# Kernel tuning notes

Hardware: AMD Instinct MI355X
Metric: run time of the kernel (lower is better)

The kernel has to match this reference:

```python
import jax, jax.numpy as jnp
import numpy as np

VAR_NUM, IN_DIM, OUT_DIM = 3, 8, 32
N_PTS, M_PTS, K_LAST = 8192, 2048, 10
RADIUS = 0.0342
PROJ_HIDDEN = 64
N_DIM = 2
MLP_DIMS = [2 * N_DIM + OUT_DIM, 80, 80, OUT_DIM]  # [36, 80, 80, 32]


def _gelu(x):
    # torch F.gelu default = exact erf form
    return jax.nn.gelu(x, approximate=False)


def _radius_neighbors(data, queries, r):
    # CSR-style neighbor lists (indices grouped per query), chunked for memory
    idx_chunks = []
    counts = np.zeros(queries.shape[0], np.int64)
    r2 = r * r
    for s in range(0, queries.shape[0], 1024):
        q = queries[s:s + 1024]
        d2 = ((q[:, None, :] - data[None, :, :]) ** 2).sum(-1)
        mask = d2 <= r2
        _, cols = np.nonzero(mask)  # row-major -> grouped by query
        idx_chunks.append(cols.astype(np.int32))
        counts[s:s + q.shape[0]] = mask.sum(1)
    return np.concatenate(idx_chunks), counts.astype(np.int32)


def _knn(data, queries, k):
    out = np.zeros((queries.shape[0], k), np.int32)
    for s in range(0, queries.shape[0], 1024):
        q = queries[s:s + 1024]
        d2 = ((q[:, None, :] - data[None, :, :]) ** 2).sum(-1)
        out[s:s + q.shape[0]] = np.argpartition(d2, k, axis=1)[:, :k]
    return out.reshape(-1)


def _mlp_params(key, dims):
    Ws, bs = [], []
    for i in range(len(dims) - 1):
        key, k1 = jax.random.split(key)
        Ws.append(jax.random.normal(k1, (dims[i], dims[i + 1]), jnp.float32) / np.sqrt(dims[i]).astype(np.float32))
        bs.append(jnp.zeros((dims[i + 1],), jnp.float32))
    return Ws, bs


def setup_inputs():
    rng = np.random.default_rng(0)
    input_grid = rng.uniform(size=(N_PTS, N_DIM)).astype(np.float32)
    output_grid = rng.uniform(size=(M_PTS, N_DIM)).astype(np.float32)
    nbr_index, nbr_counts = _radius_neighbors(input_grid, input_grid, RADIUS)
    nbr_seg = np.repeat(np.arange(N_PTS, dtype=np.int32), nbr_counts)
    nbr_last_index = _knn(input_grid, output_grid, K_LAST)

    key = jax.random.key(0)
    ks = jax.random.split(key, 4)
    inp = jax.random.normal(ks[0], (1, N_PTS, VAR_NUM * IN_DIM), jnp.float32)
    pW, pb = _mlp_params(ks[1], [IN_DIM, PROJ_HIDDEN, OUT_DIM])
    it0_W, it0_b = _mlp_params(ks[2], MLP_DIMS)
    it1_W, it1_b = _mlp_params(ks[3], MLP_DIMS)
    return dict(
        inp=inp,
        input_grid=jnp.asarray(input_grid), output_grid=jnp.asarray(output_grid),
        proj_W0=pW[0], proj_b0=pb[0], proj_W1=pW[1], proj_b1=pb[1],
        it0_W0=it0_W[0], it0_b0=it0_b[0], it0_W1=it0_W[1], it0_b1=it0_b[1], it0_W2=it0_W[2], it0_b2=it0_b[2],
        it1_W0=it1_W[0], it1_b0=it1_b[0], it1_W1=it1_W[1], it1_b1=it1_b[1], it1_W2=it1_W[2], it1_b2=it1_b[2],
        nbr_index=jnp.asarray(nbr_index), nbr_seg=jnp.asarray(nbr_seg),
        nbr_counts=jnp.asarray(nbr_counts), nbr_last_index=jnp.asarray(nbr_last_index),
    )


def _mlp3(x, W0, b0, W1, b1, W2, b2):
    x = _gelu(x @ W0 + b0)
    x = _gelu(x @ W1 + b1)
    return x @ W2 + b2


def reference(inp, input_grid, output_grid, proj_W0, proj_b0, proj_W1, proj_b1,
              it0_W0, it0_b0, it0_W1, it0_b1, it0_W2, it0_b2,
              it1_W0, it1_b0, it1_W1, it1_b1, it1_W2, it1_b2,
              nbr_index, nbr_seg, nbr_counts, nbr_last_index):
    B, N, _ = inp.shape  # B must be 1 (module's IT indexing assumes it)
    x = inp.reshape(B * N, VAR_NUM, IN_DIM)
    # pointwise projection MLP (gelu between layers)
    x = _gelu(x @ proj_W0 + proj_b0) @ proj_W1 + proj_b1  # (N, V, OUT_DIM)

    inv_counts = (1.0 / jnp.maximum(nbr_counts, 1).astype(x.dtype))[:, None]
    y_pos = input_grid[nbr_index]        # (E, 2) neighbor positions
    self_pos = input_grid[nbr_seg]       # (E, 2) query positions
    last_y = input_grid[nbr_last_index]                    # (M*K, 2)
    last_self = jnp.repeat(output_grid, K_LAST, axis=0)    # (M*K, 2)

    outs = []
    for v in range(VAR_NUM):
        f = x[:, v, :]
        # IT layer 0: radius neighborhoods on input grid, residual add
        agg = jnp.concatenate([y_pos, self_pos, f[nbr_index]], axis=-1)  # (E, 36)
        h = _mlp3(agg, it0_W0, it0_b0, it0_W1, it0_b1, it0_W2, it0_b2)
        f = jax.ops.segment_sum(h, nbr_seg, num_segments=N) * inv_counts + f
        # IT layer 1 (last): fixed-K neighbors from input grid to output grid, mean
        agg = jnp.concatenate([last_y, last_self, f[nbr_last_index]], axis=-1)
        h = _mlp3(agg, it1_W0, it1_b0, it1_W1, it1_b1, it1_W2, it1_b2)
        outs.append(h.reshape(M_PTS, K_LAST, OUT_DIM).mean(axis=1))
    # original concatenates temp[None] along dim=2 -> (1, M, V*OUT_DIM)
    return jnp.concatenate(outs, axis=-1)[None]
```

## Files before the change

kernel.cpp:

```cpp
#include <hip/hip_runtime.h>
#include <hip/hip_bf16.h>
#include <math.h>

#define N_PTS 8192
#define M_PTS 2048
#define KLAST 10
#define VARS 3
#define OUTD 32
#define D1 80
#define D2 80
#define PB 8
#define LPTS 4
#define NT 512
#define NWAVES 8
#define NTL 256
#define NWL 4
#define TPCH 104
#define RP 32

#define FRAG 512
#define W0F 10
#define W1F 15
#define W2F 6
#define WPACK ((W0F + W1F + W2F) * FRAG)

typedef float f4 __attribute__((ext_vector_type(4)));
typedef short bf16x8 __attribute__((ext_vector_type(8)));

__device__ __forceinline__ float gelu_f(float x) {
    float x2 = x * x;
    float s = x * __builtin_fmaf(0.1029418f, x2, 2.3022083f);
    float u = __builtin_amdgcn_exp2f(s);
    float r = __builtin_amdgcn_rcpf(u + 1.0f);
    return __builtin_fmaf(-x, r, x);
}
__device__ __forceinline__ unsigned short f2bf(float x) {
    unsigned int u = __float_as_uint(x);
    u += 0x7FFF + ((u >> 16) & 1);
    return (unsigned short)(u >> 16);
}
__device__ __forceinline__ float bf2f(unsigned short h) {
    return __uint_as_float(((unsigned int)h) << 16);
}
__device__ __forceinline__ int pk2(float a, float b) {
    __hip_bfloat162 h = __float22bfloat162_rn(float2{a, b});
    int r; __builtin_memcpy(&r, &h, 4); return r;
}

__device__ __forceinline__ void pack_weights(
    const float* __restrict__ W0g, const float* __restrict__ W1g,
    const float* __restrict__ W2g, unsigned short* __restrict__ wp, int t)
{
    for (int idx = t; idx < W0F * FRAG; idx += 256) {
        int f = idx >> 9, r = idx & 511;
        int lane = r >> 3, e = r & 7;
        int lm = lane & 15, quad = lane >> 4;
        int cb = f >> 1, ks = f & 1;
        int col = cb * 16 + lm;
        int k = ks * 32 + quad * 8 + e;
        float w = (k < 32) ? W0g[(k + 4) * D1 + col]
                           : ((k < 36) ? W0g[(k - 32) * D1 + col] : 0.0f);
        wp[idx] = f2bf(w);
    }
    for (int idx = t; idx < W1F * FRAG; idx += 256) {
        int f = idx >> 9, r = idx & 511;
        int lane = r >> 3, e = r & 7;
        int lm = lane & 15, quad = lane >> 4;
        int cb = f / 3, ks = f - cb * 3;
        int col = cb * 16 + lm;
        int k = ks * 32 + quad * 8 + e;
        wp[W0F * FRAG + idx] = f2bf((k < D2) ? W1g[k * D1 + col] : 0.0f);
    }
    for (int idx = t; idx < W2F * FRAG; idx += 256) {
        int f = idx >> 9, r = idx & 511;
        int lane = r >> 3, e = r & 7;
        int lm = lane & 15, quad = lane >> 4;
        int cb = f / 3, ks = f - cb * 3;
        int col = cb * 16 + lm;
        int k = ks * 32 + quad * 8 + e;
        wp[(W0F + W1F) * FRAG + idx] = f2bf((k < D2) ? W2g[k * OUTD + col] : 0.0f);
    }
}

__device__ __forceinline__ void mlp_chunk(
    int4 featsi, int4 posfi, unsigned short* Trow,
    const unsigned short* __restrict__ Wl,
    const float* bs, int lm, int quad)
{
    bf16x8 b1f0 = *(bf16x8*)&featsi;
    bf16x8 b1f1 = *(bf16x8*)&posfi;
#pragma unroll 1
    for (int cb = 0; cb < 5; ++cb) {
        f4 acc = *(const f4*)&bs[cb * 16 + quad * 4];
        bf16x8 a0 = *(const bf16x8*)&Wl[(cb * 2 + 0) * FRAG];
        bf16x8 a1 = *(const bf16x8*)&Wl[(cb * 2 + 1) * FRAG];
        acc = __builtin_amdgcn_mfma_f32_16x16x32_bf16(a0, b1f0, acc, 0, 0, 0);
        acc = __builtin_amdgcn_mfma_f32_16x16x32_bf16(a1, b1f1, acc, 0, 0, 0);
        *(int2*)&Trow[cb * 16 + quad * 4] =
            make_int2(pk2(gelu_f(acc.x), gelu_f(acc.y)),
                      pk2(gelu_f(acc.z), gelu_f(acc.w)));
    }
    bf16x8 b2f[3];
    b2f[0] = *(const bf16x8*)&Trow[quad * 8];
    b2f[1] = *(const bf16x8*)&Trow[32 + quad * 8];
    b2f[2] = *(const bf16x8*)&Trow[64 + quad * 8];
#pragma unroll 1
    for (int cb = 0; cb < 5; ++cb) {
        f4 acc = *(const f4*)&bs[80 + cb * 16 + quad * 4];
        const unsigned short* wh = &Wl[(W0F + cb * 3) * FRAG];
        bf16x8 h0 = *(const bf16x8*)&wh[0];
        bf16x8 h1 = *(const bf16x8*)&wh[FRAG];
        bf16x8 h2 = *(const bf16x8*)&wh[2 * FRAG];
        acc = __builtin_amdgcn_mfma_f32_16x16x32_bf16(h0, b2f[0], acc, 0, 0, 0);
        acc = __builtin_amdgcn_mfma_f32_16x16x32_bf16(h1, b2f[1], acc, 0, 0, 0);
        acc = __builtin_amdgcn_mfma_f32_16x16x32_bf16(h2, b2f[2], acc, 0, 0, 0);
        *(int2*)&Trow[cb * 16 + quad * 4] =
            make_int2(pk2(gelu_f(acc.x), gelu_f(acc.y)),
                      pk2(gelu_f(acc.z), gelu_f(acc.w)));
    }
    bf16x8 b3f[3];
    b3f[0] = *(const bf16x8*)&Trow[quad * 8];
    b3f[1] = *(const bf16x8*)&Trow[32 + quad * 8];
    b3f[2] = *(const bf16x8*)&Trow[64 + quad * 8];
    float* po = (float*)Trow;
#pragma unroll 1
    for (int cb = 0; cb < 2; ++cb) {
        f4 acc = *(const f4*)&bs[160 + cb * 16 + quad * 4];
        const unsigned short* wh = &Wl[(W0F + W1F + cb * 3) * FRAG];
        bf16x8 h0 = *(const bf16x8*)&wh[0];
        bf16x8 h1 = *(const bf16x8*)&wh[FRAG];
        bf16x8 h2 = *(const bf16x8*)&wh[2 * FRAG];
        acc = __builtin_amdgcn_mfma_f32_16x16x32_bf16(h0, b3f[0], acc, 0, 0, 0);
        acc = __builtin_amdgcn_mfma_f32_16x16x32_bf16(h1, b3f[1], acc, 0, 0, 0);
        acc = __builtin_amdgcn_mfma_f32_16x16x32_bf16(h2, b3f[2], acc, 0, 0, 0);
        *(f4*)&po[cb * 16 + quad * 4] = acc;
    }
}

__global__ __launch_bounds__(256) void proj_scan_kernel(
    const float* __restrict__ inp, const float* __restrict__ grid_in,
    const float* __restrict__ W0, const float* __restrict__ b0,
    const float* __restrict__ W1, const float* __restrict__ b1,
    unsigned short* __restrict__ f0b, int* __restrict__ posb,
    const int* __restrict__ counts, int* __restrict__ offsets,
    const float* __restrict__ i0W0, const float* __restrict__ i0W1,
    const float* __restrict__ i0W2, unsigned short* __restrict__ wpack0,
    const float* __restrict__ i1W0, const float* __restrict__ i1W1,
    const float* __restrict__ i1W2, unsigned short* __restrict__ wpack1)
{
    const int t = threadIdx.x;
    if (blockIdx.x == 769) { pack_weights(i0W0, i0W1, i0W2, wpack0, t); return; }
    if (blockIdx.x == 770) { pack_weights(i1W0, i1W1, i1W2, wpack1, t); return; }
    if (blockIdx.x == 768) {
        __shared__ int ws2[4], wx2[4];
        const int lane = t & 63, wave = t >> 6;
        int4 a[8];
#pragma unroll
        for (int i = 0; i < 8; ++i) a[i] = ((const int4*)counts)[t * 8 + i];
        int s = 0;
#pragma unroll
        for (int i = 0; i < 8; ++i) s += a[i].x + a[i].y + a[i].z + a[i].w;
        int x = s;
#pragma unroll
        for (int d = 1; d < 64; d <<= 1) {
            int y = __shfl_up(x, d);
            if (lane >= d) x += y;
        }
        if (lane == 63) ws2[wave] = x;
        __syncthreads();
        if (t == 0) {
            wx2[0] = 0;
            wx2[1] = ws2[0];
            wx2[2] = ws2[0] + ws2[1];
            wx2[3] = ws2[0] + ws2[1] + ws2[2];
        }
        __syncthreads();
        int base = wx2[wave] + (x - s);
#pragma unroll
        for (int i = 0; i < 8; ++i) {
            int4 c = a[i];
            int4 o;
            o.x = base; base += c.x;
            o.y = base; base += c.y;
            o.z = base; base += c.z;
            o.w = base; base += c.w;
            ((int4*)offsets)[t * 8 + i] = o;
        }
        return;
    }
    __shared__ float W0s[8 * 64];
    __shared__ float W1s[64 * OUTD];
    __shared__ float xs[32 * 8];
    __shared__ float H[32 * 64];
    const int r0 = blockIdx.x * 32;
    for (int idx = t; idx < 512; idx += 256) W0s[idx] = W0[idx];
    for (int idx = t; idx < 64 * OUTD; idx += 256) W1s[idx] = W1[idx];
    xs[t] = inp[r0 * 8 + t];
    if (t < 32) {
        int row = r0 + t, n = row / 3;
        posb[n] = pk2(grid_in[2 * n], grid_in[2 * n + 1]);
    }
    __syncthreads();
#pragma unroll 1
    for (int p = 0; p < 8; ++p) {
        int o = t + 256 * p, r = o >> 6, col = o & 63;
        float s = b0[col];
#pragma unroll
        for (int k = 0; k < 8; ++k) s += xs[r * 8 + k] * W0s[k * 64 + col];
        H[o] = gelu_f(s);
    }
    __syncthreads();
#pragma unroll 1
    for (int p = 0; p < 4; ++p) {
        int o = t + 256 * p, r = o >> 5, c = o & 31;
        float s = b1[c];
#pragma unroll 8
        for (int k = 0; k < 64; ++k) s += H[r * 64 + k] * W1s[k * OUTD + c];
        int row = r0 + r;
        int n = row / 3, v = row - n * 3;
        f0b[((size_t)(v << 13) + n) * RP + c] = f2bf(s);
    }
}

__global__ __launch_bounds__(512, 8) void agg_kernel(
    const float* __restrict__ grid_in, const unsigned short* __restrict__ f0b,
    const int* __restrict__ posb,
    const int* __restrict__ nbr_index, const int* __restrict__ offsets,
    const int* __restrict__ counts,
    const unsigned short* __restrict__ wpack,
    const float* __restrict__ b0g, const float* __restrict__ b1g,
    const float* __restrict__ b2g,
    unsigned short* __restrict__ f1b)
{
    __shared__ __attribute__((aligned(16))) unsigned short Tb[NWAVES * 16 * TPCH];
    __shared__ __attribute__((aligned(16))) float bs[192];
    __shared__ __attribute__((aligned(16))) float accH[VARS * PB * 32];
    __shared__ int offs[PB + 1];
    __shared__ int px2b[PB];
    __shared__ float invb[PB];

    const int t = threadIdx.x;
    const int lane = t & 63, wave = t >> 6;
    const int lm = lane & 15, quad = lane >> 4;
    const int p0 = blockIdx.x * PB;
    const unsigned short* Wl = wpack + lane * 8;

    for (int idx = t; idx < 192; idx += NT)
        bs[idx] = (idx < 80) ? b0g[idx] : (idx < 160 ? b1g[idx - 80] : b2g[idx - 160]);
    if (t < PB) {
        offs[t] = offsets[p0 + t];
        int c = counts[p0 + t];
        invb[t] = 1.0f / (float)(c > 1 ? c : 1);
        px2b[t] = pk2(grid_in[2 * (p0 + t)], grid_in[2 * (p0 + t) + 1]);
    }
    if (t == PB) offs[PB] = offsets[p0 + PB - 1] + counts[p0 + PB - 1];
    for (int idx = t; idx < VARS * PB * 32; idx += NT) accH[idx] = 0.0f;
    __syncthreads();

    unsigned short* TbW = Tb + (wave * 16) * TPCH;
    if (lane < 32)
        *(int4*)(TbW + (lane >> 1) * TPCH + 80 + (lane & 1) * 8) = make_int4(0, 0, 0, 0);

    const int e0 = offs[0];
    const int cntT = offs[PB] - e0;
    const int Rb = VARS * cntT;
    const int nch = (Rb + 15) >> 4;

    unsigned short* Trow = TbW + lm * TPCH;

    auto fetch_index = [&](int ch2, int& key, int& j) {
        key = -1; j = 0;
        if (ch2 < nch) {
            int myrow = (ch2 << 4) + lm;
            if (myrow < Rb) {
                int myv = (myrow >= 2 * cntT) ? 2 : ((myrow >= cntT) ? 1 : 0);
                int e = e0 + myrow - myv * cntT;
                int lp = 0;
#pragma unroll
                for (int l = 1; l < PB; ++l) lp += (e >= offs[l]);
                key = myv * PB + lp;
                j = nbr_index[e];
            }
        }
    };
    auto fetch_record = [&](int key, int j, int4& feats, int4& posf) {
        feats = make_int4(0, 0, 0, 0); posf = make_int4(0, 0, 0, 0);
        if (key >= 0) {
            int v = key >> 3, lp = key & 7;
            feats = ((const int4*)(f0b + ((size_t)(v << 13) + j) * RP))[quad];
            if (quad == 0) posf = make_int4(posb[j], px2b[lp], 0, 0);
        }
    };

    int keyA, jA, keyB, jB;
    fetch_index(wave, keyA, jA);
    fetch_index(wave + NWAVES, keyB, jB);
    int4 featsA, posfA;
    fetch_record(keyA, jA, featsA, posfA);

    for (int ch = wave; ch < nch; ch += NWAVES) {
        int ckey = keyA; int4 cf = featsA, cp = posfA;
        keyA = keyB; jA = jB;
        fetch_index(ch + 2 * NWAVES, keyB, jB);
        fetch_record(keyA, jA, featsA, posfA);
        mlp_chunk(cf, cp, Trow, Wl, bs, lm, quad);
        int col = lane & 31, eo = lane >> 5;
#pragma unroll 1
        for (int e2 = eo; e2 < 16; e2 += 2) {
            int k = __shfl(ckey, e2);
            if (k >= 0)
                atomicAdd(&accH[k * 32 + col], ((const float*)(TbW + e2 * TPCH))[col]);
        }
    }
    __syncthreads();
    for (int idx = t; idx < VARS * PB * OUTD; idx += NT) {
        int key = idx >> 5, c = idx & 31;
        int v = key >> 3, lp = key & 7;
        size_t rec = ((size_t)(v << 13) + p0 + lp) * RP;
        float val = accH[key * 32 + c] * invb[lp] + bf2f(f0b[rec + c]);
        f1b[rec + c] = f2bf(val);
    }
}

__global__ __launch_bounds__(256, 8) void last_kernel(
    const unsigned short* __restrict__ f1b, const int* __restrict__ posb,
    const float* __restrict__ grid_out,
    const int* __restrict__ nbr_last,
    const unsigned short* __restrict__ wpack,
    const float* __restrict__ b0g, const float* __restrict__ b1g,
    const float* __restrict__ b2g,
    float* __restrict__ out)
{
    __shared__ __attribute__((aligned(16))) unsigned short Tb[NWL * 16 * TPCH];
    __shared__ __attribute__((aligned(16))) float bs[192];
    __shared__ __attribute__((aligned(16))) float accH[LPTS * VARS * 32];
    __shared__ int pxo2b[LPTS];

    const int t = threadIdx.x;
    const int lane = t & 63, wave = t >> 6;
    const int lm = lane & 15, quad = lane >> 4;
    const int m0 = blockIdx.x * LPTS;
    const unsigned short* Wl = wpack + lane * 8;

    for (int idx = t; idx < 192; idx += NTL)
        bs[idx] = (idx < 80) ? b0g[idx] : (idx < 160 ? b1g[idx - 80] : b2g[idx - 160]);
    if (t < LPTS)
        pxo2b[t] = pk2(grid_out[2 * (m0 + t)], grid_out[2 * (m0 + t) + 1]);
    for (int idx = t; idx < LPTS * VARS * 32; idx += NTL) accH[idx] = 0.0f;
    __syncthreads();
    unsigned short* TbW = Tb + (wave * 16) * TPCH;
    if (lane < 32)
        *(int4*)(TbW + (lane >> 1) * TPCH + 80 + (lane & 1) * 8) = make_int4(0, 0, 0, 0);

    const int Rb = LPTS * VARS * KLAST;
    const int nch = (Rb + 15) >> 4;
    unsigned short* Trow = TbW + lm * TPCH;

    auto fetch_index = [&](int ch2, int& key, int& j) {
        key = -1; j = 0;
        if (ch2 < nch) {
            int myrow = (ch2 << 4) + lm;
            if (myrow < Rb) {
                int lp = myrow / 30, rr = myrow - lp * 30;
                int v = rr / KLAST, kk = rr - v * KLAST;
                j = nbr_last[(m0 + lp) * KLAST + kk];
                key = lp * VARS + v;
            }
        }
    };
    auto fetch_record = [&](int key, int j, int4& feats, int4& posf) {
        feats = make_int4(0, 0, 0, 0); posf = make_int4(0, 0, 0, 0);
        if (key >= 0) {
            int lp = key / VARS, v = key - lp * VARS;
            feats = ((const int4*)(f1b + ((size_t)(v << 13) + j) * RP))[quad];
            if (quad == 0) posf = make_int4(posb[j], pxo2b[lp], 0, 0);
        }
    };

    int keyA, jA, keyB, jB;
    fetch_index(wave, keyA, jA);
    fetch_index(wave + NWL, keyB, jB);
    int4 featsA, posfA;
    fetch_record(keyA, jA, featsA, posfA);

    for (int ch = wave; ch < nch; ch += NWL) {
        int ckey = keyA; int4 cf = featsA, cp = posfA;
        keyA = keyB; jA = jB;
        fetch_index(ch + 2 * NWL, keyB, jB);
        fetch_record(keyA, jA, featsA, posfA);
        mlp_chunk(cf, cp, Trow, Wl, bs, lm, quad);
        int col = lane & 31, eo = lane >> 5;
#pragma unroll 1
        for (int e2 = eo; e2 < 16; e2 += 2) {
            int k = __shfl(ckey, e2);
            if (k >= 0)
                atomicAdd(&accH[k * 32 + col], ((const float*)(TbW + e2 * TPCH))[col]);
        }
    }
    __syncthreads();
    for (int idx = t; idx < LPTS * VARS * OUTD; idx += NTL) {
        int key = idx >> 5, c = idx & 31;
        int lp = key / VARS, v = key - lp * VARS;
        out[((size_t)(m0 + lp) * VARS + v) * OUTD + c] = accH[key * 32 + c] * (1.0f / KLAST);
    }
}

extern "C" void kernel_launch(void* const* d_in, const int* in_sizes, int n_in,
                              void* d_out, int out_size, void* d_ws, size_t ws_size,
                              hipStream_t stream) {
    const float* inp      = (const float*)d_in[0];
    const float* grid_in  = (const float*)d_in[1];
    const float* grid_out = (const float*)d_in[2];
    const float* pW0 = (const float*)d_in[3];
    const float* pb0 = (const float*)d_in[4];
    const float* pW1 = (const float*)d_in[5];
    const float* pb1 = (const float*)d_in[6];
    const float* i0W0 = (const float*)d_in[7];
    const float* i0b0 = (const float*)d_in[8];
    const float* i0W1 = (const float*)d_in[9];
    const float* i0b1 = (const float*)d_in[10];
    const float* i0W2 = (const float*)d_in[11];
    const float* i0b2 = (const float*)d_in[12];
    const float* i1W0 = (const float*)d_in[13];
    const float* i1b0 = (const float*)d_in[14];
    const float* i1W1 = (const float*)d_in[15];
    const float* i1b1 = (const float*)d_in[16];
    const float* i1W2 = (const float*)d_in[17];
    const float* i1b2 = (const float*)d_in[18];
    const int* nbr_index  = (const int*)d_in[19];
    const int* nbr_counts = (const int*)d_in[21];
    const int* nbr_last   = (const int*)d_in[22];

    unsigned short* f0b = (unsigned short*)d_ws;
    unsigned short* f1b = f0b + (size_t)VARS * N_PTS * RP;
    int* offsets = (int*)(f1b + (size_t)VARS * N_PTS * RP);
    int* posb    = offsets + N_PTS;
    unsigned short* wpack0 = (unsigned short*)(posb + N_PTS);
    unsigned short* wpack1 = wpack0 + WPACK;

    proj_scan_kernel<<<771, 256, 0, stream>>>(inp, grid_in, pW0, pb0, pW1, pb1,
                                              f0b, posb, nbr_counts, offsets,
                                              i0W0, i0W1, i0W2, wpack0,
                                              i1W0, i1W1, i1W2, wpack1);
    agg_kernel<<<N_PTS / PB, NT, 0, stream>>>(grid_in, f0b, posb, nbr_index, offsets,
                                              nbr_counts, wpack0,
                                              i0b0, i0b1, i0b2, f1b);
    last_kernel<<<M_PTS / LPTS, NTL, 0, stream>>>(f1b, posb, grid_out, nbr_last, wpack1,
                                                  i1b0, i1b1, i1b2,
                                                  (float*)d_out);
}
```

Measured before the change: 308.9 us.

## Keep MLP activations in registers and stage packed weights in LDS

The MLP chunk no longer round-trips layer activations through an LDS scratch tile. The weight packing order is permuted so each MFMA output fragment maps directly onto the next layer's B-operand registers. The final layer atomically adds its accumulator straight into a transposed, padded shared accumulator, replacing the shuffle-and-atomic loop. Packed weights are copied into LDS per block instead of being read from global memory, and the output kernel now handles 2 points per block instead of 4. In exchange, every block pays a larger LDS footprint and a weight copy, which may reduce occupancy.

```diff
diff --git a/kernel.cpp b/kernel.cpp
--- a/kernel.cpp
+++ b/kernel.cpp
@@ -10,12 +10,11 @@
 #define D1 80
 #define D2 80
 #define PB 8
-#define LPTS 4
+#define LPTS 2
 #define NT 512
 #define NWAVES 8
 #define NTL 256
 #define NWL 4
-#define TPCH 104
 #define RP 32
 
 #define FRAG 512
@@ -23,6 +22,11 @@
 #define W1F 15
 #define W2F 6
 #define WPACK ((W0F + W1F + W2F) * FRAG)
+
+#define AKEYS (VARS * PB)
+#define AKP   (AKEYS + 1)
+#define LKEYS (LPTS * VARS)
+#define LKP   (LKEYS + 1)
 
 typedef float f4 __attribute__((ext_vector_type(4)));
 typedef short bf16x8 __attribute__((ext_vector_type(8)));
@@ -45,6 +49,10 @@
 __device__ __forceinline__ int pk2(float a, float b) {
     __hip_bfloat162 h = __float22bfloat162_rn(float2{a, b});
     int r; __builtin_memcpy(&r, &h, 4); return r;
+}
+__device__ __forceinline__ bf16x8 mk8(int a, int b, int c, int d) {
+    int4 v = make_int4(a, b, c, d);
+    bf16x8 r; __builtin_memcpy(&r, &v, 16); return r;
 }
 
 __device__ __forceinline__ void pack_weights(
@@ -54,10 +62,10 @@
     for (int idx = t; idx < W0F * FRAG; idx += 256) {
         int f = idx >> 9, r = idx & 511;
         int lane = r >> 3, e = r & 7;
-        int lm = lane & 15, quad = lane >> 4;
+        int lm = lane & 15, qd = lane >> 4;
         int cb = f >> 1, ks = f & 1;
         int col = cb * 16 + lm;
-        int k = ks * 32 + quad * 8 + e;
+        int k = ks * 32 + qd * 8 + e;
         float w = (k < 32) ? W0g[(k + 4) * D1 + col]
                            : ((k < 36) ? W0g[(k - 32) * D1 + col] : 0.0f);
         wp[idx] = f2bf(w);
@@ -65,76 +73,87 @@
     for (int idx = t; idx < W1F * FRAG; idx += 256) {
         int f = idx >> 9, r = idx & 511;
         int lane = r >> 3, e = r & 7;
-        int lm = lane & 15, quad = lane >> 4;
+        int lm = lane & 15, qd = lane >> 4;
         int cb = f / 3, ks = f - cb * 3;
         int col = cb * 16 + lm;
-        int k = ks * 32 + quad * 8 + e;
-        wp[W0F * FRAG + idx] = f2bf((k < D2) ? W1g[k * D1 + col] : 0.0f);
+        int blk = 2 * ks + (e >> 2);
+        int srow = blk * 16 + qd * 4 + (e & 3);
+        wp[W0F * FRAG + idx] = f2bf((blk < 5) ? W1g[srow * D1 + col] : 0.0f);
     }
     for (int idx = t; idx < W2F * FRAG; idx += 256) {
         int f = idx >> 9, r = idx & 511;
         int lane = r >> 3, e = r & 7;
-        int lm = lane & 15, quad = lane >> 4;
+        int lm = lane & 15, qd = lane >> 4;
         int cb = f / 3, ks = f - cb * 3;
         int col = cb * 16 + lm;
-        int k = ks * 32 + quad * 8 + e;
-        wp[(W0F + W1F) * FRAG + idx] = f2bf((k < D2) ? W2g[k * OUTD + col] : 0.0f);
-    }
-}
+        int blk = 2 * ks + (e >> 2);
+        int srow = blk * 16 + qd * 4 + (e & 3);
+        wp[(W0F + W1F) * FRAG + idx] = f2bf((blk < 5) ? W2g[srow * OUTD + col] : 0.0f);
+    }
+}
+
+#define MFMA16(A, B, C) __builtin_amdgcn_mfma_f32_16x16x32_bf16(A, B, C, 0, 0, 0)
+#define GPACK(ACC) make_int2(pk2(gelu_f(ACC.x), gelu_f(ACC.y)), \
+                             pk2(gelu_f(ACC.z), gelu_f(ACC.w)))
 
 __device__ __forceinline__ void mlp_chunk(
-    int4 featsi, int4 posfi, unsigned short* Trow,
-    const unsigned short* __restrict__ Wl,
-    const float* bs, int lm, int quad)
+    int4 featsi, int2 posfi,
+    const unsigned short* WA, const float* bs,
+    int quad, int ckey, float* accH, int kp)
 {
-    bf16x8 b1f0 = *(bf16x8*)&featsi;
-    bf16x8 b1f1 = *(bf16x8*)&posfi;
-#pragma unroll 1
-    for (int cb = 0; cb < 5; ++cb) {
-        f4 acc = *(const f4*)&bs[cb * 16 + quad * 4];
-        bf16x8 a0 = *(const bf16x8*)&Wl[(cb * 2 + 0) * FRAG];
-        bf16x8 a1 = *(const bf16x8*)&Wl[(cb * 2 + 1) * FRAG];
-        acc = __builtin_amdgcn_mfma_f32_16x16x32_bf16(a0, b1f0, acc, 0, 0, 0);
-        acc = __builtin_amdgcn_mfma_f32_16x16x32_bf16(a1, b1f1, acc, 0, 0, 0);
-        *(int2*)&Trow[cb * 16 + quad * 4] =
-            make_int2(pk2(gelu_f(acc.x), gelu_f(acc.y)),
-                      pk2(gelu_f(acc.z), gelu_f(acc.w)));
-    }
-    bf16x8 b2f[3];
-    b2f[0] = *(const bf16x8*)&Trow[quad * 8];
-    b2f[1] = *(const bf16x8*)&Trow[32 + quad * 8];
-    b2f[2] = *(const bf16x8*)&Trow[64 + quad * 8];
-#pragma unroll 1
-    for (int cb = 0; cb < 5; ++cb) {
-        f4 acc = *(const f4*)&bs[80 + cb * 16 + quad * 4];
-        const unsigned short* wh = &Wl[(W0F + cb * 3) * FRAG];
-        bf16x8 h0 = *(const bf16x8*)&wh[0];
-        bf16x8 h1 = *(const bf16x8*)&wh[FRAG];
-        bf16x8 h2 = *(const bf16x8*)&wh[2 * FRAG];
-        acc = __builtin_amdgcn_mfma_f32_16x16x32_bf16(h0, b2f[0], acc, 0, 0, 0);
-        acc = __builtin_amdgcn_mfma_f32_16x16x32_bf16(h1, b2f[1], acc, 0, 0, 0);
-        acc = __builtin_amdgcn_mfma_f32_16x16x32_bf16(h2, b2f[2], acc, 0, 0, 0);
-        *(int2*)&Trow[cb * 16 + quad * 4] =
-            make_int2(pk2(gelu_f(acc.x), gelu_f(acc.y)),
-                      pk2(gelu_f(acc.z), gelu_f(acc.w)));
-    }
-    bf16x8 b3f[3];
-    b3f[0] = *(const bf16x8*)&Trow[quad * 8];
-    b3f[1] = *(const bf16x8*)&Trow[32 + quad * 8];
-    b3f[2] = *(const bf16x8*)&Trow[64 + quad * 8];
-    float* po = (float*)Trow;
-#pragma unroll 1
-    for (int cb = 0; cb < 2; ++cb) {
-        f4 acc = *(const f4*)&bs[160 + cb * 16 + quad * 4];
-        const unsigned short* wh = &Wl[(W0F + W1F + cb * 3) * FRAG];
-        bf16x8 h0 = *(const bf16x8*)&wh[0];
-        bf16x8 h1 = *(const bf16x8*)&wh[FRAG];
-        bf16x8 h2 = *(const bf16x8*)&wh[2 * FRAG];
-        acc = __builtin_amdgcn_mfma_f32_16x16x32_bf16(h0, b3f[0], acc, 0, 0, 0);
-        acc = __builtin_amdgcn_mfma_f32_16x16x32_bf16(h1, b3f[1], acc, 0, 0, 0);
-        acc = __builtin_amdgcn_mfma_f32_16x16x32_bf16(h2, b3f[2], acc, 0, 0, 0);
-        *(f4*)&po[cb * 16 + quad * 4] = acc;
-    }
+    bf16x8 b1f0; __builtin_memcpy(&b1f0, &featsi, 16);
+    int4 pv = make_int4(posfi.x, posfi.y, 0, 0);
+    bf16x8 b1f1; __builtin_memcpy(&b1f1, &pv, 16);
+
+    int2 k0, k1, k2, k3, k4;
+#define L1S(CB, PK) { \
+    f4 acc = *(const f4*)&bs[(CB) * 16 + quad * 4]; \
+    bf16x8 a0 = *(const bf16x8*)&WA[((CB) * 2 + 0) * FRAG]; \
+    bf16x8 a1 = *(const bf16x8*)&WA[((CB) * 2 + 1) * FRAG]; \
+    acc = MFMA16(a0, b1f0, acc); \
+    acc = MFMA16(a1, b1f1, acc); \
+    PK = GPACK(acc); }
+    L1S(0, k0) L1S(1, k1) L1S(2, k2) L1S(3, k3) L1S(4, k4)
+#undef L1S
+
+    bf16x8 b20 = mk8(k0.x, k0.y, k1.x, k1.y);
+    bf16x8 b21 = mk8(k2.x, k2.y, k3.x, k3.y);
+    bf16x8 b22 = mk8(k4.x, k4.y, 0, 0);
+    int2 q0, q1, q2, q3, q4;
+#define L2S(CB, QK) { \
+    f4 acc = *(const f4*)&bs[80 + (CB) * 16 + quad * 4]; \
+    const unsigned short* wh = &WA[(W0F + (CB) * 3) * FRAG]; \
+    bf16x8 h0 = *(const bf16x8*)&wh[0]; \
+    bf16x8 h1 = *(const bf16x8*)&wh[FRAG]; \
+    bf16x8 h2 = *(const bf16x8*)&wh[2 * FRAG]; \
+    acc = MFMA16(h0, b20, acc); \
+    acc = MFMA16(h1, b21, acc); \
+    acc = MFMA16(h2, b22, acc); \
+    QK = GPACK(acc); }
+    L2S(0, q0) L2S(1, q1) L2S(2, q2) L2S(3, q3) L2S(4, q4)
+#undef L2S
+
+    bf16x8 b30 = mk8(q0.x, q0.y, q1.x, q1.y);
+    bf16x8 b31 = mk8(q2.x, q2.y, q3.x, q3.y);
+    bf16x8 b32 = mk8(q4.x, q4.y, 0, 0);
+#define L3S(CB) { \
+    f4 acc = *(const f4*)&bs[160 + (CB) * 16 + quad * 4]; \
+    const unsigned short* wh = &WA[(W0F + W1F + (CB) * 3) * FRAG]; \
+    bf16x8 h0 = *(const bf16x8*)&wh[0]; \
+    bf16x8 h1 = *(const bf16x8*)&wh[FRAG]; \
+    bf16x8 h2 = *(const bf16x8*)&wh[2 * FRAG]; \
+    acc = MFMA16(h0, b30, acc); \
+    acc = MFMA16(h1, b31, acc); \
+    acc = MFMA16(h2, b32, acc); \
+    if (ckey >= 0) { \
+        float* ap = accH + ((CB) * 16 + quad * 4) * kp + ckey; \
+        atomicAdd(&ap[0], acc.x); \
+        atomicAdd(&ap[kp], acc.y); \
+        atomicAdd(&ap[2 * kp], acc.z); \
+        atomicAdd(&ap[3 * kp], acc.w); \
+    } }
+    L3S(0) L3S(1)
+#undef L3S
 }
 
 __global__ __launch_bounds__(256) void proj_scan_kernel(
@@ -232,18 +251,22 @@
     const float* __restrict__ b2g,
     unsigned short* __restrict__ f1b)
 {
-    __shared__ __attribute__((aligned(16))) unsigned short Tb[NWAVES * 16 * TPCH];
+    __shared__ __attribute__((aligned(16))) unsigned short Wls[WPACK];
     __shared__ __attribute__((aligned(16))) float bs[192];
-    __shared__ __attribute__((aligned(16))) float accH[VARS * PB * 32];
+    __shared__ __attribute__((aligned(16))) float accH[OUTD * AKP];
     __shared__ int offs[PB + 1];
     __shared__ int px2b[PB];
     __shared__ float invb[PB];
 
     const int t = threadIdx.x;
-    const int lane = t & 63, wave = t >> 6;
+    const int lane = t & 63;
     const int lm = lane & 15, quad = lane >> 4;
+    const int wave = t >> 6;
     const int p0 = blockIdx.x * PB;
-    const unsigned short* Wl = wpack + lane * 8;
+
+    for (int idx = t; idx < WPACK / 8; idx += NT)
+        ((int4*)Wls)[idx] = ((const int4*)wpack)[idx];
+    const unsigned short* WA = Wls + lane * 8;
 
     for (int idx = t; idx < 192; idx += NT)
         bs[idx] = (idx < 80) ? b0g[idx] : (idx < 160 ? b1g[idx - 80] : b2g[idx - 160]);
@@ -254,19 +277,13 @@
         px2b[t] = pk2(grid_in[2 * (p0 + t)], grid_in[2 * (p0 + t) + 1]);
     }
     if (t == PB) offs[PB] = offsets[p0 + PB - 1] + counts[p0 + PB - 1];
-    for (int idx = t; idx < VARS * PB * 32; idx += NT) accH[idx] = 0.0f;
-    __syncthreads();
-
-    unsigned short* TbW = Tb + (wave * 16) * TPCH;
-    if (lane < 32)
-        *(int4*)(TbW + (lane >> 1) * TPCH + 80 + (lane & 1) * 8) = make_int4(0, 0, 0, 0);
+    for (int idx = t; idx < OUTD * AKP; idx += NT) accH[idx] = 0.0f;
+    __syncthreads();
 
     const int e0 = offs[0];
     const int cntT = offs[PB] - e0;
     const int Rb = VARS * cntT;
     const int nch = (Rb + 15) >> 4;
-
-    unsigned short* Trow = TbW + lm * TPCH;
 
     auto fetch_index = [&](int ch2, int& key, int& j) {
         key = -1; j = 0;
@@ -283,41 +300,34 @@
             }
         }
     };
-    auto fetch_record = [&](int key, int j, int4& feats, int4& posf) {
-        feats = make_int4(0, 0, 0, 0); posf = make_int4(0, 0, 0, 0);
+    auto fetch_record = [&](int key, int j, int4& feats, int2& posf) {
+        feats = make_int4(0, 0, 0, 0); posf = make_int2(0, 0);
         if (key >= 0) {
             int v = key >> 3, lp = key & 7;
             feats = ((const int4*)(f0b + ((size_t)(v << 13) + j) * RP))[quad];
-            if (quad == 0) posf = make_int4(posb[j], px2b[lp], 0, 0);
+            if (quad == 0) posf = make_int2(posb[j], px2b[lp]);
         }
     };
 
     int keyA, jA, keyB, jB;
     fetch_index(wave, keyA, jA);
     fetch_index(wave + NWAVES, keyB, jB);
-    int4 featsA, posfA;
+    int4 featsA; int2 posfA;
     fetch_record(keyA, jA, featsA, posfA);
 
     for (int ch = wave; ch < nch; ch += NWAVES) {
-        int ckey = keyA; int4 cf = featsA, cp = posfA;
+        int ckey = keyA; int4 cf = featsA; int2 cp = posfA;
         keyA = keyB; jA = jB;
         fetch_index(ch + 2 * NWAVES, keyB, jB);
         fetch_record(keyA, jA, featsA, posfA);
-        mlp_chunk(cf, cp, Trow, Wl, bs, lm, quad);
-        int col = lane & 31, eo = lane >> 5;
-#pragma unroll 1
-        for (int e2 = eo; e2 < 16; e2 += 2) {
-            int k = __shfl(ckey, e2);
-            if (k >= 0)
-                atomicAdd(&accH[k * 32 + col], ((const float*)(TbW + e2 * TPCH))[col]);
-        }
+        mlp_chunk(cf, cp, WA, bs, quad, ckey, accH, AKP);
     }
     __syncthreads();
     for (int idx = t; idx < VARS * PB * OUTD; idx += NT) {
         int key = idx >> 5, c = idx & 31;
         int v = key >> 3, lp = key & 7;
         size_t rec = ((size_t)(v << 13) + p0 + lp) * RP;
-        float val = accH[key * 32 + c] * invb[lp] + bf2f(f0b[rec + c]);
+        float val = accH[c * AKP + key] * invb[lp] + bf2f(f0b[rec + c]);
         f1b[rec + c] = f2bf(val);
     }
 }
@@ -331,30 +341,30 @@
     const float* __restrict__ b2g,
     float* __restrict__ out)
 {
-    __shared__ __attribute__((aligned(16))) unsigned short Tb[NWL * 16 * TPCH];
+    __shared__ __attribute__((aligned(16))) unsigned short Wls[WPACK];
     __shared__ __attribute__((aligned(16))) float bs[192];
-    __shared__ __attribute__((aligned(16))) float accH[LPTS * VARS * 32];
+    __shared__ __attribute__((aligned(16))) float accH[OUTD * LKP];
     __shared__ int pxo2b[LPTS];
 
     const int t = threadIdx.x;
-    const int lane = t & 63, wave = t >> 6;
+    const int lane = t & 63;
     const int lm = lane & 15, quad = lane >> 4;
+    const int wave = t >> 6;
     const int m0 = blockIdx.x * LPTS;
-    const unsigned short* Wl = wpack + lane * 8;
+
+    for (int idx = t; idx < WPACK / 8; idx += NTL)
+        ((int4*)Wls)[idx] = ((const int4*)wpack)[idx];
+    const unsigned short* WA = Wls + lane * 8;
 
     for (int idx = t; idx < 192; idx += NTL)
         bs[idx] = (idx < 80) ? b0g[idx] : (idx < 160 ? b1g[idx - 80] : b2g[idx - 160]);
     if (t < LPTS)
         pxo2b[t] = pk2(grid_out[2 * (m0 + t)], grid_out[2 * (m0 + t) + 1]);
-    for (int idx = t; idx < LPTS * VARS * 32; idx += NTL) accH[idx] = 0.0f;
-    __syncthreads();
-    unsigned short* TbW = Tb + (wave * 16) * TPCH;
-    if (lane < 32)
-        *(int4*)(TbW + (lane >> 1) * TPCH + 80 + (lane & 1) * 8) = make_int4(0, 0, 0, 0);
+    for (int idx = t; idx < OUTD * LKP; idx += NTL) accH[idx] = 0.0f;
+    __syncthreads();
 
     const int Rb = LPTS * VARS * KLAST;
     const int nch = (Rb + 15) >> 4;
-    unsigned short* Trow = TbW + lm * TPCH;
 
     auto fetch_index = [&](int ch2, int& key, int& j) {
         key = -1; j = 0;
@@ -368,40 +378,34 @@
             }
         }
     };
-    auto fetch_record = [&](int key, int j, int4& feats, int4& posf) {
-        feats = make_int4(0, 0, 0, 0); posf = make_int4(0, 0, 0, 0);
+    auto fetch_record = [&](int key, int j, int4& feats, int2& posf) {
+        feats = make_int4(0, 0, 0, 0); posf = make_int2(0, 0);
         if (key >= 0) {
             int lp = key / VARS, v = key - lp * VARS;
             feats = ((const int4*)(f1b + ((size_t)(v << 13) + j) * RP))[quad];
-            if (quad == 0) posf = make_int4(posb[j], pxo2b[lp], 0, 0);
+            if (quad == 0) posf = make_int2(posb[j], pxo2b[lp]);
         }
     };
 
     int keyA, jA, keyB, jB;
     fetch_index(wave, keyA, jA);
     fetch_index(wave + NWL, keyB, jB);
-    int4 featsA, posfA;
+    int4 featsA; int2 posfA;
     fetch_record(keyA, jA, featsA, posfA);
 
     for (int ch = wave; ch < nch; ch += NWL) {
-        int ckey = keyA; int4 cf = featsA, cp = posfA;
+        int ckey = keyA; int4 cf = featsA; int2 cp = posfA;
         keyA = keyB; jA = jB;
         fetch_index(ch + 2 * NWL, keyB, jB);
         fetch_record(keyA, jA, featsA, posfA);
-        mlp_chunk(cf, cp, Trow, Wl, bs, lm, quad);
-        int col = lane & 31, eo = lane >> 5;
-#pragma unroll 1
-        for (int e2 = eo; e2 < 16; e2 += 2) {
-            int k = __shfl(ckey, e2);
-            if (k >= 0)
-                atomicAdd(&accH[k * 32 + col], ((const float*)(TbW + e2 * TPCH))[col]);
-        }
+        mlp_chunk(cf, cp, WA, bs, quad, ckey, accH, LKP);
     }
     __syncthreads();
     for (int idx = t; idx < LPTS * VARS * OUTD; idx += NTL) {
         int key = idx >> 5, c = idx & 31;
         int lp = key / VARS, v = key - lp * VARS;
-        out[((size_t)(m0 + lp) * VARS + v) * OUTD + c] = accH[key * 32 + c] * (1.0f / KLAST);
+        out[((size_t)(m0 + lp) * VARS + v) * OUTD + c] =
+            accH[c * LKP + key] * (1.0f / KLAST);
     }
 }
 
```

After: 577.0 us. 1.87x slower.
